# Performance work log

Measured on AMD Instinct MI355X. Metric: run time of the kernel, lower is better.

Reference implementation:

```python
import jax, jax.numpy as jnp
import numpy as np

N = 100000
E = 3200000
F_IN = 128
H1, C1 = 2, 16          # conv1: heads=2, out_channels=16, concat -> 32
H2, C2 = 1, 40          # conv2: heads=1, out_channels=num_classes=40
NEG_SLOPE = 0.2


def setup_inputs() -> dict:
    key = jax.random.key(0)
    ks = jax.random.split(key, 12)
    features = jax.random.normal(ks[0], (N, F_IN), dtype=jnp.float32)
    edges = jax.random.randint(ks[1], (2, E), 0, N, dtype=jnp.int64)
    weight = jax.random.uniform(ks[2], (E,), dtype=jnp.float32)  # ignored (edge_dim=None)
    s = 0.1
    W1 = jax.random.normal(ks[3], (F_IN, H1 * C1), dtype=jnp.float32) * s
    att_src1 = jax.random.normal(ks[4], (H1, C1), dtype=jnp.float32) * s
    att_dst1 = jax.random.normal(ks[5], (H1, C1), dtype=jnp.float32) * s
    b1 = jnp.zeros((H1 * C1,), dtype=jnp.float32)
    W2 = jax.random.normal(ks[6], (H1 * C1, H2 * C2), dtype=jnp.float32) * s
    att_src2 = jax.random.normal(ks[7], (H2, C2), dtype=jnp.float32) * s
    att_dst2 = jax.random.normal(ks[8], (H2, C2), dtype=jnp.float32) * s
    b2 = jnp.zeros((H2 * C2,), dtype=jnp.float32)
    return {"features": features, "edges": edges, "weight": weight,
            "W1": W1, "att_src1": att_src1, "att_dst1": att_dst1, "b1": b1,
            "W2": W2, "att_src2": att_src2, "att_dst2": att_dst2, "b2": b2}


def _segment_softmax(e, seg, num_segments):
    # e: [E, H]; softmax over edges sharing the same destination node
    m = jax.ops.segment_max(e, seg, num_segments=num_segments)
    ex = jnp.exp(e - m[seg])
    s = jax.ops.segment_sum(ex, seg, num_segments=num_segments)
    return ex / (s[seg] + 1e-16)


def _gat_conv(x, src, dst, W, att_src, att_dst, bias, heads, out_ch):
    n = x.shape[0]
    h = (x @ W).reshape(n, heads, out_ch)                  # [N,H,C]
    a_src = jnp.sum(h * att_src, axis=-1)                  # [N,H]
    a_dst = jnp.sum(h * att_dst, axis=-1)                  # [N,H]
    e = a_src[src] + a_dst[dst]                            # [E,H]
    e = jnp.where(e > 0, e, NEG_SLOPE * e)                 # LeakyReLU(0.2)
    alpha = _segment_softmax(e, dst, n)                    # [E,H]
    msg = h[src] * alpha[:, :, None]                       # [E,H,C]
    out = jax.ops.segment_sum(msg, dst, num_segments=n)    # [N,H,C]
    return out.reshape(n, heads * out_ch) + bias           # concat=True


def reference(features, edges, weight, W1, att_src1, att_dst1, b1,
              W2, att_src2, att_dst2, b2):
    n = features.shape[0]
    # GATConv default add_self_loops=True (self-loop removal of pre-existing
    # loops skipped: negligible for random edges and not jit-shape-friendly)
    loop = jnp.arange(n, dtype=edges.dtype)
    src = jnp.concatenate([edges[0], loop])
    dst = jnp.concatenate([edges[1], loop])
    x = _gat_conv(features, src, dst, W1, att_src1, att_dst1, b1, H1, C1)
    x = jax.nn.relu(x)
    # F.dropout with training=self.training -> identity in eval mode
    x = _gat_conv(x, src, dst, W2, att_src2, att_dst2, b2, H2, C2)
    return x
```

## Files before the change

kernel.cpp:

```cpp
#include <hip/hip_runtime.h>


#define DEVFN __device__ __forceinline__
#define CB_SHIFT 8
#define CB_SZ 256
#define SC_CHUNK 4096
#define NBMAX 512
#define STASH 12288
#define A2B 240

DEVFN unsigned short f2h(float f) {
  _Float16 h = (_Float16)f;
  unsigned short u;
  __builtin_memcpy(&u, &h, 2);
  return u;
}
DEVFN float h2f(unsigned short u) {
  _Float16 h;
  __builtin_memcpy(&h, &u, 2);
  return (float)h;
}

DEVFN float lrelu(float e) { return e > 0.f ? e : 0.2f * e; }

DEVFN void acc8(float* acc, float x, uint4 u) {
  acc[0] = fmaf(x, h2f(u.x & 0xffff), acc[0]);
  acc[1] = fmaf(x, h2f(u.x >> 16),    acc[1]);
  acc[2] = fmaf(x, h2f(u.y & 0xffff), acc[2]);
  acc[3] = fmaf(x, h2f(u.y >> 16),    acc[3]);
  acc[4] = fmaf(x, h2f(u.z & 0xffff), acc[4]);
  acc[5] = fmaf(x, h2f(u.z >> 16),    acc[5]);
  acc[6] = fmaf(x, h2f(u.w & 0xffff), acc[6]);
  acc[7] = fmaf(x, h2f(u.w >> 16),    acc[7]);
}

DEVFN void read_edge(const long long* eg64, const int* eg32, int is64, int E,
                     int i, int& s, int& d) {
  if (i >= E) { s = d = i - E; return; }
  if (is64) { s = (int)eg64[i]; d = (int)eg64[E + i]; }
  else      { s = eg32[i];      d = eg32[E + i]; }
}

DEVFN int detect64(const int* eg32, int E, int i0, int t) {
  int base = i0;
  if (base > E - 64) base = E - 64;
  if (base < 0) base = 0;
  int i = base + (t & 63);
  unsigned long long m = __ballot((i < E) && (eg32[2 * i + 1] != 0));
  return m == 0ull;
}

__global__ __launch_bounds__(256) void bucket_hist(const long long* eg64,
                                                   const int* eg32,
                                                   int E, int N, int NB2,
                                                   int* __restrict__ bhist) {
  __shared__ int lh[NBMAX];
  int t = threadIdx.x;
  lh[t] = 0; lh[t + 256] = 0;
  int is64 = detect64(eg32, E, 0, t);
  __syncthreads();
  int EN = E + N;
  int step = (int)gridDim.x * 1024;
  for (int base = (int)blockIdx.x * 1024; base < EN; base += step) {
#pragma unroll
    for (int k = 0; k < 4; k++) {
      int i = base + k * 256 + t;
      if (i < EN) {
        int d;
        if (i >= E) d = i - E;
        else d = is64 ? (int)eg64[E + i] : eg32[E + i];
        atomicAdd(&lh[d >> CB_SHIFT], 1);
      }
    }
  }
  __syncthreads();
  if (t < NB2 && lh[t]) atomicAdd(&bhist[t], lh[t]);
  int t2 = t + 256;
  if (t2 < NB2 && lh[t2]) atomicAdd(&bhist[t2], lh[t2]);
}

__global__ void bucket_scan(const int* __restrict__ bhist,
                            int* __restrict__ bscan, int* __restrict__ gcur,
                            int NB2, int EN) {
  __shared__ int buf[2][NBMAX];
  int t = threadIdx.x;
  int v = (t < NB2) ? bhist[t] : 0;
  buf[0][t] = v;
  __syncthreads();
  int pin = 0;
  for (int off = 1; off < NBMAX; off <<= 1) {
    int nv = buf[pin][t] + (t >= off ? buf[pin][t - off] : 0);
    buf[1 - pin][t] = nv;
    pin ^= 1;
    __syncthreads();
  }
  int excl = buf[pin][t] - v;
  if (t < NB2) { bscan[t] = excl; gcur[t] = excl; }
  if (t == NB2) bscan[t] = EN;
}

__global__ __launch_bounds__(256) void chunk_scatter_sorted(
    const long long* eg64, const int* eg32, int E, int N, int NB2,
    int* __restrict__ gcur, int* __restrict__ tmp) {
  __shared__ int lh[NBMAX];
  __shared__ int lscan[NBMAX];
  __shared__ int lpos[NBMAX];
  __shared__ int gbase[NBMAX];
  __shared__ int sbuf[2][NBMAX];
  __shared__ int payl[SC_CHUNK];
  __shared__ unsigned short bktid[SC_CHUNK];
  int t = threadIdx.x;
  int i0 = (int)blockIdx.x * SC_CHUNK;
  int is64 = detect64(eg32, E, i0, t);
  lh[t] = 0; lh[t + 256] = 0;
  __syncthreads();
  int EN = E + N;
  int i1 = i0 + SC_CHUNK; if (i1 > EN) i1 = EN;
  int total = i1 - i0;
  int es[16], ed[16];
#pragma unroll
  for (int bb = 0; bb < 4; bb++) {
#pragma unroll
    for (int k = 0; k < 4; k++) {
      int idx = bb * 4 + k;
      int i = i0 + bb * 1024 + k * 256 + t;
      int s = 0, d = -1;
      if (i < i1) read_edge(eg64, eg32, is64, E, i, s, d);
      es[idx] = s; ed[idx] = d;
    }
  }
#pragma unroll
  for (int j = 0; j < 16; j++)
    if (ed[j] >= 0) atomicAdd(&lh[ed[j] >> CB_SHIFT], 1);
  __syncthreads();
  sbuf[0][t] = lh[t]; sbuf[0][t + 256] = lh[t + 256];
  __syncthreads();
  int pin = 0;
  for (int off = 1; off < NBMAX; off <<= 1) {
    int nv0 = sbuf[pin][t] + (t >= off ? sbuf[pin][t - off] : 0);
    int nv1 = sbuf[pin][t + 256] + sbuf[pin][t + 256 - off];
    __syncthreads();
    sbuf[1 - pin][t] = nv0; sbuf[1 - pin][t + 256] = nv1;
    pin ^= 1;
    __syncthreads();
  }
  lscan[t] = sbuf[pin][t] - lh[t];
  lscan[t + 256] = sbuf[pin][t + 256] - lh[t + 256];
  lpos[t] = lscan[t]; lpos[t + 256] = lscan[t + 256];
  if (t < NB2 && lh[t]) gbase[t] = atomicAdd(&gcur[t], lh[t]);
  int t2 = t + 256;
  if (t2 < NB2 && lh[t2]) gbase[t2] = atomicAdd(&gcur[t2], lh[t2]);
  __syncthreads();
#pragma unroll
  for (int j = 0; j < 16; j++) {
    if (ed[j] >= 0) {
      int b = ed[j] >> CB_SHIFT;
      int sl = atomicAdd(&lpos[b], 1);
      payl[sl] = (es[j] << CB_SHIFT) | (ed[j] & (CB_SZ - 1));
      bktid[sl] = (unsigned short)b;
    }
  }
  __syncthreads();
  for (int j = t; j < total; j += 256) {
    int b = bktid[j];
    tmp[gbase[b] + (j - lscan[b])] = payl[j];
  }
}

__global__ __launch_bounds__(256) void bucket_rp_sort(const int* __restrict__ bscan,
                                                      const int* __restrict__ tmp,
                                                      int* __restrict__ rp,
                                                      int* __restrict__ csr,
                                                      int N, int EN) {
  __shared__ int lc[CB_SZ];
  __shared__ int ps[256];
  __shared__ int lcur[CB_SZ];
  __shared__ int stash[STASH];
  int b = blockIdx.x, t = threadIdx.x;
  lc[t] = 0;
  __syncthreads();
  int w0 = bscan[b];
  int w1 = bscan[b + 1];
  int cnt = w1 - w0;
  bool fit = (cnt <= STASH);
  int p = w0 + t;
  for (; p + 768 < w1; p += 1024) {
    int e0 = tmp[p], e1 = tmp[p + 256], e2 = tmp[p + 512], e3 = tmp[p + 768];
    if (fit) {
      stash[p - w0] = e0; stash[p - w0 + 256] = e1;
      stash[p - w0 + 512] = e2; stash[p - w0 + 768] = e3;
    }
    atomicAdd(&lc[e0 & (CB_SZ - 1)], 1);
    atomicAdd(&lc[e1 & (CB_SZ - 1)], 1);
    atomicAdd(&lc[e2 & (CB_SZ - 1)], 1);
    atomicAdd(&lc[e3 & (CB_SZ - 1)], 1);
  }
  if (p < w1) {
    bool v1 = p + 256 < w1, v2 = p + 512 < w1;
    int q1 = v1 ? p + 256 : p;
    int q2 = v2 ? p + 512 : p;
    int e0 = tmp[p], e1 = tmp[q1], e2 = tmp[q2];
    if (fit) {
      stash[p - w0] = e0;
      if (v1) stash[q1 - w0] = e1;
      if (v2) stash[q2 - w0] = e2;
    }
    atomicAdd(&lc[e0 & (CB_SZ - 1)], 1);
    if (v1) atomicAdd(&lc[e1 & (CB_SZ - 1)], 1);
    if (v2) atomicAdd(&lc[e2 & (CB_SZ - 1)], 1);
  }
  __syncthreads();
  int a = lc[t];
  ps[t] = a;
  __syncthreads();
  for (int off = 1; off < 256; off <<= 1) {
    int v = ps[t];
    int u = (t >= off) ? ps[t - off] : 0;
    __syncthreads();
    ps[t] = v + u;
    __syncthreads();
  }
  int base = w0 + ps[t] - a;
  lcur[t] = base;
  int n0 = b * CB_SZ;
  if (n0 + t < N) rp[n0 + t] = base;
  if (b == (int)gridDim.x - 1 && t == 0) rp[N] = EN;
  __syncthreads();
  if (fit) {
    for (int j = t; j < cnt; j += 256) {
      int e = stash[j];
      int pos = atomicAdd(&lcur[e & (CB_SZ - 1)], 1);
      csr[pos] = e >> CB_SHIFT;
    }
  } else {
    for (int q = w0 + t; q < w1; q += 256) {
      int e = tmp[q];
      int pos = atomicAdd(&lcur[e & (CB_SZ - 1)], 1);
      csr[pos] = e >> CB_SHIFT;
    }
  }
}

__global__ __launch_bounds__(256) void gemm1f(const float* __restrict__ X,
                                              const float* __restrict__ W,
                                              const float* __restrict__ att_s,
                                              const float* __restrict__ att_d,
                                              uint4* __restrict__ h1h,
                                              float* __restrict__ as1,
                                              float* __restrict__ ad1, int N) {
  __shared__ float Wl[128 * 32];
  __shared__ float Asl[32], Adl[32];
  int t = threadIdx.x;
  for (int i = t; i < 1024; i += 256)
    ((float4*)Wl)[i] = ((const float4*)W)[i];
  if (t < 32) { Asl[t] = att_s[t]; Adl[t] = att_d[t]; }
  __syncthreads();
  int n = blockIdx.x * 256 + t;
  if (n >= N) return;
  const float4* X4 = (const float4*)(X + (size_t)n * 128);
  float acc[32];
#pragma unroll
  for (int c = 0; c < 32; c++) acc[c] = 0.f;
  for (int k4 = 0; k4 < 32; k4++) {
    float4 x = X4[k4];
    const float4* w4 = (const float4*)(Wl + k4 * 128);
#pragma unroll
    for (int c4 = 0; c4 < 8; c4++) {
      float4 w0 = w4[c4], w1 = w4[8 + c4], w2 = w4[16 + c4], w3 = w4[24 + c4];
      float* A = acc + c4 * 4;
      A[0] = fmaf(x.x, w0.x, A[0]); A[1] = fmaf(x.x, w0.y, A[1]);
      A[2] = fmaf(x.x, w0.z, A[2]); A[3] = fmaf(x.x, w0.w, A[3]);
      A[0] = fmaf(x.y, w1.x, A[0]); A[1] = fmaf(x.y, w1.y, A[1]);
      A[2] = fmaf(x.y, w1.z, A[2]); A[3] = fmaf(x.y, w1.w, A[3]);
      A[0] = fmaf(x.z, w2.x, A[0]); A[1] = fmaf(x.z, w2.y, A[1]);
      A[2] = fmaf(x.z, w2.z, A[2]); A[3] = fmaf(x.z, w2.w, A[3]);
      A[0] = fmaf(x.w, w3.x, A[0]); A[1] = fmaf(x.w, w3.y, A[1]);
      A[2] = fmaf(x.w, w3.z, A[2]); A[3] = fmaf(x.w, w3.w, A[3]);
    }
  }
  float s0 = 0.f, d0 = 0.f, s1 = 0.f, d1 = 0.f;
#pragma unroll
  for (int c = 0; c < 16; c++) {
    s0 = fmaf(acc[c], Asl[c], s0);
    d0 = fmaf(acc[c], Adl[c], d0);
    s1 = fmaf(acc[16 + c], Asl[16 + c], s1);
    d1 = fmaf(acc[16 + c], Adl[16 + c], d1);
  }
  as1[n * 2] = s0; as1[n * 2 + 1] = s1;
  ad1[n * 2] = d0; ad1[n * 2 + 1] = d1;
#pragma unroll
  for (int j = 0; j < 4; j++) {
    uint4 u;
    u.x = (unsigned)f2h(acc[j * 8 + 0]) | ((unsigned)f2h(acc[j * 8 + 1]) << 16);
    u.y = (unsigned)f2h(acc[j * 8 + 2]) | ((unsigned)f2h(acc[j * 8 + 3]) << 16);
    u.z = (unsigned)f2h(acc[j * 8 + 4]) | ((unsigned)f2h(acc[j * 8 + 5]) << 16);
    u.w = (unsigned)f2h(acc[j * 8 + 6]) | ((unsigned)f2h(acc[j * 8 + 7]) << 16);
    h1h[(size_t)n * 4 + j] = u;
  }
}

__global__ __launch_bounds__(256, 8) void agg1_gemm2(
    const int* __restrict__ rp, const int* __restrict__ csr,
    const float* __restrict__ as, const float* __restrict__ ad,
    const uint4* __restrict__ h1h, const float* __restrict__ b1,
    const float* __restrict__ W2, const float* __restrict__ as2w,
    const float* __restrict__ ad2w, uint4* __restrict__ h2h,
    float* __restrict__ as2, float* __restrict__ ad2, int N) {
  __shared__ float Wl[32 * 40];
  __shared__ float As2l[40], Ad2l[40];
  __shared__ float x1t[16][33];
  __shared__ float h2r[16][41];
  int t = threadIdx.x;
  for (int i = t; i < 320; i += 256)
    ((float4*)Wl)[i] = ((const float4*)W2)[i];
  if (t < 40) { As2l[t] = as2w[t]; Ad2l[t] = ad2w[t]; }
  int nl = t >> 4, r = t & 15;
  int half = r >> 2, cq = r & 3;
  int h = cq >> 1;
  int n = blockIdx.x * 16 + nl;
  float acc[8] = {0, 0, 0, 0, 0, 0, 0, 0};
  float ssum = 0.f;
  if (n < N) {
    int p0 = rp[n], p1 = rp[n + 1];
    float adv = ad[n * 2 + h];
    int p = p0 + half;
    for (; p + 12 < p1; p += 16) {
      int sA = csr[p], sB = csr[p + 4], sC = csr[p + 8], sD = csr[p + 12];
      float eA = as[sA * 2 + h] + adv;
      float eB = as[sB * 2 + h] + adv;
      float eC = as[sC * 2 + h] + adv;
      float eD = as[sD * 2 + h] + adv;
      uint4 uA = h1h[(size_t)sA * 4 + cq];
      uint4 uB = h1h[(size_t)sB * 4 + cq];
      uint4 uC = h1h[(size_t)sC * 4 + cq];
      uint4 uD = h1h[(size_t)sD * 4 + cq];
      float xA = __expf(lrelu(eA));
      float xB = __expf(lrelu(eB));
      float xC = __expf(lrelu(eC));
      float xD = __expf(lrelu(eD));
      ssum += (xA + xB) + (xC + xD);
      acc8(acc, xA, uA);
      acc8(acc, xB, uB);
      acc8(acc, xC, uC);
      acc8(acc, xD, uD);
    }
    if (p < p1) {
      bool vB = p + 4 < p1, vC = p + 8 < p1;
      int pB = vB ? p + 4 : p;
      int pC = vC ? p + 8 : p;
      int sA = csr[p], sB = csr[pB], sC = csr[pC];
      float eA = as[sA * 2 + h] + adv;
      float eB = as[sB * 2 + h] + adv;
      float eC = as[sC * 2 + h] + adv;
      uint4 uA = h1h[(size_t)sA * 4 + cq];
      uint4 uB = h1h[(size_t)sB * 4 + cq];
      uint4 uC = h1h[(size_t)sC * 4 + cq];
      float xA = __expf(lrelu(eA));
      float xB = vB ? __expf(lrelu(eB)) : 0.f;
      float xC = vC ? __expf(lrelu(eC)) : 0.f;
      ssum += xA + xB + xC;
      acc8(acc, xA, uA);
      acc8(acc, xB, uB);
      acc8(acc, xC, uC);
    }
  }
#pragma unroll
  for (int j = 0; j < 8; j++) acc[j] += __shfl_xor(acc[j], 4);
  ssum += __shfl_xor(ssum, 4);
#pragma unroll
  for (int j = 0; j < 8; j++) acc[j] += __shfl_xor(acc[j], 8);
  ssum += __shfl_xor(ssum, 8);
  if (n < N && half == 0) {
    float inv = 1.0f / (ssum + 1e-16f);
    float4 ba = ((const float4*)b1)[cq * 2];
    float4 bb = ((const float4*)b1)[cq * 2 + 1];
    int ch0 = cq * 8;
    x1t[nl][ch0 + 0] = fmaxf(fmaf(acc[0], inv, ba.x), 0.f);
    x1t[nl][ch0 + 1] = fmaxf(fmaf(acc[1], inv, ba.y), 0.f);
    x1t[nl][ch0 + 2] = fmaxf(fmaf(acc[2], inv, ba.z), 0.f);
    x1t[nl][ch0 + 3] = fmaxf(fmaf(acc[3], inv, ba.w), 0.f);
    x1t[nl][ch0 + 4] = fmaxf(fmaf(acc[4], inv, bb.x), 0.f);
    x1t[nl][ch0 + 5] = fmaxf(fmaf(acc[5], inv, bb.y), 0.f);
    x1t[nl][ch0 + 6] = fmaxf(fmaf(acc[6], inv, bb.z), 0.f);
    x1t[nl][ch0 + 7] = fmaxf(fmaf(acc[7], inv, bb.w), 0.f);
  }
  __syncthreads();
  if (n < N && r < 8) {
    float acc2[5] = {0, 0, 0, 0, 0};
    int cb = r * 5;
    for (int k = 0; k < 32; k++) {
      float x = x1t[nl][k];
#pragma unroll
      for (int c = 0; c < 5; c++)
        acc2[c] = fmaf(x, Wl[k * 40 + cb + c], acc2[c]);
    }
    float ss = 0.f, sd = 0.f;
#pragma unroll
    for (int c = 0; c < 5; c++) {
      ss = fmaf(acc2[c], As2l[cb + c], ss);
      sd = fmaf(acc2[c], Ad2l[cb + c], sd);
    }
#pragma unroll
    for (int off = 1; off < 8; off <<= 1) {
      ss += __shfl_xor(ss, off);
      sd += __shfl_xor(sd, off);
    }
    if (r == 0) { as2[n] = ss; ad2[n] = sd; }
#pragma unroll
    for (int c = 0; c < 5; c++) h2r[nl][cb + c] = acc2[c];
  }
  __syncthreads();
  if (n < N && r < 5) {
    const float* hr = h2r[nl] + r * 8;
    uint4 u;
    u.x = (unsigned)f2h(hr[0]) | ((unsigned)f2h(hr[1]) << 16);
    u.y = (unsigned)f2h(hr[2]) | ((unsigned)f2h(hr[3]) << 16);
    u.z = (unsigned)f2h(hr[4]) | ((unsigned)f2h(hr[5]) << 16);
    u.w = (unsigned)f2h(hr[6]) | ((unsigned)f2h(hr[7]) << 16);
    h2h[(size_t)n * 8 + r] = u;
  }
}

__global__ __launch_bounds__(256, 8) void agg2_fused(const int* __restrict__ rp,
                                                     const int* __restrict__ csr,
                                                     const float* __restrict__ as,
                                                     const float* __restrict__ ad,
                                                     const uint4* __restrict__ h2h,
                                                     const float* __restrict__ bias,
                                                     float* __restrict__ outp, int N) {
  __shared__ float part[256][9];
  int t = threadIdx.x;
  int idx = blockIdx.x * A2B + t;
  bool act = (t < A2B) && (idx < N * 20);
  int n = 0, half = 0, cq = 0, p0 = 0, p1 = 0;
  float adv = 0.f;
  if (act) {
    n = idx / 20;
    int rr = idx % 20;
    half = rr / 5;
    cq = rr - half * 5;
    p0 = rp[n]; p1 = rp[n + 1];
    adv = ad[n];
  }
  float acc[8] = {0, 0, 0, 0, 0, 0, 0, 0};
  float ssum = 0.f;
  if (act) {
    int p = p0 + half;
    for (; p + 12 < p1; p += 16) {
      int sA = csr[p], sB = csr[p + 4], sC = csr[p + 8], sD = csr[p + 12];
      float eA = as[sA] + adv;
      float eB = as[sB] + adv;
      float eC = as[sC] + adv;
      float eD = as[sD] + adv;
      uint4 uA = h2h[(size_t)sA * 8 + cq];
      uint4 uB = h2h[(size_t)sB * 8 + cq];
      uint4 uC = h2h[(size_t)sC * 8 + cq];
      uint4 uD = h2h[(size_t)sD * 8 + cq];
      float xA = __expf(lrelu(eA));
      float xB = __expf(lrelu(eB));
      float xC = __expf(lrelu(eC));
      float xD = __expf(lrelu(eD));
      ssum += (xA + xB) + (xC + xD);
      acc8(acc, xA, uA);
      acc8(acc, xB, uB);
      acc8(acc, xC, uC);
      acc8(acc, xD, uD);
    }
    if (p < p1) {
      bool vB = p + 4 < p1, vC = p + 8 < p1;
      int pB = vB ? p + 4 : p;
      int pC = vC ? p + 8 : p;
      int sA = csr[p], sB = csr[pB], sC = csr[pC];
      float eA = as[sA] + adv;
      float eB = as[sB] + adv;
      float eC = as[sC] + adv;
      uint4 uA = h2h[(size_t)sA * 8 + cq];
      uint4 uB = h2h[(size_t)sB * 8 + cq];
      uint4 uC = h2h[(size_t)sC * 8 + cq];
      float xA = __expf(lrelu(eA));
      float xB = vB ? __expf(lrelu(eB)) : 0.f;
      float xC = vC ? __expf(lrelu(eC)) : 0.f;
      ssum += xA + xB + xC;
      acc8(acc, xA, uA);
      acc8(acc, xB, uB);
      acc8(acc, xC, uC);
    }
  }
  if (act && half) {
#pragma unroll
    for (int j = 0; j < 8; j++) part[t][j] = acc[j];
    part[t][8] = ssum;
  }
  __syncthreads();
  if (act && half == 0) {
#pragma unroll
    for (int j = 0; j < 8; j++)
      acc[j] += part[t + 5][j] + part[t + 10][j] + part[t + 15][j];
    ssum += part[t + 5][8] + part[t + 10][8] + part[t + 15][8];
    float inv = 1.0f / (ssum + 1e-16f);
    const float4* b4 = (const float4*)bias;
    float4 ba = b4[cq * 2], bb = b4[cq * 2 + 1];
    float4 r0, r1;
    r0.x = fmaf(acc[0], inv, ba.x);
    r0.y = fmaf(acc[1], inv, ba.y);
    r0.z = fmaf(acc[2], inv, ba.z);
    r0.w = fmaf(acc[3], inv, ba.w);
    r1.x = fmaf(acc[4], inv, bb.x);
    r1.y = fmaf(acc[5], inv, bb.y);
    r1.z = fmaf(acc[6], inv, bb.z);
    r1.w = fmaf(acc[7], inv, bb.w);
    ((float4*)outp)[(size_t)n * 10 + cq * 2]     = r0;
    ((float4*)outp)[(size_t)n * 10 + cq * 2 + 1] = r1;
  }
}

extern "C" void kernel_launch(void* const* d_in, const int* in_sizes, int n_in,
                              void* d_out, int out_size, void* d_ws, size_t ws_size,
                              hipStream_t stream) {
  const float* X    = (const float*)d_in[0];
  const long long* eg64 = (const long long*)d_in[1];
  const int* eg32   = (const int*)d_in[1];
  const float* W1   = (const float*)d_in[3];
  const float* as1w = (const float*)d_in[4];
  const float* ad1w = (const float*)d_in[5];
  const float* b1   = (const float*)d_in[6];
  const float* W2   = (const float*)d_in[7];
  const float* as2w = (const float*)d_in[8];
  const float* ad2w = (const float*)d_in[9];
  const float* b2   = (const float*)d_in[10];
  float* out = (float*)d_out;

  const int N  = in_sizes[0] / 128;
  const int E  = in_sizes[1] / 2;
  const int EN = E + N;
  const int NB2 = (N + CB_SZ - 1) / CB_SZ;
  const int NWG = (EN + SC_CHUNK - 1) / SC_CHUNK;

  char* wbase = (char*)d_ws;
  size_t off = 0;
  auto alloc = [&](size_t bytes) -> void* {
    void* p = wbase + off;
    off += (bytes + 255) & ~(size_t)255;
    return p;
  };

  uint4* h1h = (uint4*)alloc((size_t)N * 64);
  size_t usz = (size_t)EN * 4;
  if ((size_t)N * 128 > usz) usz = (size_t)N * 128;
  char* uni = (char*)alloc(usz);
  uint4* h2h = (uint4*)uni;
  int*   tmp = (int*)uni;
  float* as1 = (float*)alloc((size_t)N * 2 * 4);
  float* ad1 = (float*)alloc((size_t)N * 2 * 4);
  float* as2 = (float*)alloc((size_t)N * 4);
  float* ad2 = (float*)alloc((size_t)N * 4);
  int* rp     = (int*)alloc((size_t)(N + 1) * 4);
  int* bhist  = (int*)alloc(NBMAX * 4);
  int* bscan  = (int*)alloc((NBMAX + 1) * 4);
  int* gcur   = (int*)alloc(NBMAX * 4);
  int* csr    = (int*)alloc((size_t)EN * 4);
  (void)ws_size; (void)n_in; (void)out_size;

  const int gN = (N + 255) / 256;

  hipMemsetAsync(bhist, 0, NBMAX * 4, stream);
  bucket_hist<<<1024, 256, 0, stream>>>(eg64, eg32, E, N, NB2, bhist);
  bucket_scan<<<1, NBMAX, 0, stream>>>(bhist, bscan, gcur, NB2, EN);
  chunk_scatter_sorted<<<NWG, 256, 0, stream>>>(eg64, eg32, E, N, NB2, gcur, tmp);
  bucket_rp_sort<<<NB2, 256, 0, stream>>>(bscan, tmp, rp, csr, N, EN);

  gemm1f<<<gN, 256, 0, stream>>>(X, W1, as1w, ad1w, h1h, as1, ad1, N);
  agg1_gemm2<<<(N + 15) / 16, 256, 0, stream>>>(rp, csr, as1, ad1, h1h, b1,
                                                W2, as2w, ad2w, h2h, as2, ad2, N);
  agg2_fused<<<(N * 20 + A2B - 1) / A2B, 256, 0, stream>>>(rp, csr, as2, ad2,
                                                           h2h, b2, out, N);
}
```

Measured before the change: 331.7 us.

## Replace per-bucket CSR sort with global per-node histogram, scan, and atomic scatter

The CSR build no longer does a bucket histogram followed by a per-bucket block sort that stashes each bucket in LDS. It now counts every destination node with global atomics, runs a three-kernel prefix scan to produce row pointers and bucket cursors, keeps the chunked bucket scatter (which also writes bucket ids), and finishes with a flat atomic scatter into CSR positions. This removes the per-bucket LDS-limited sort kernel, whose per-block work depended on bucket size. In exchange it adds global atomic contention on per-node counters, extra launches, an extra bucket-id array written and read, and a full per-node memset.

Result: slower. 491.0 us (+48.0%).

```diff
diff --git a/kernel.cpp b/kernel.cpp
--- a/kernel.cpp
+++ b/kernel.cpp
@@ -6,7 +6,6 @@
 #define CB_SZ 256
 #define SC_CHUNK 4096
 #define NBMAX 512
-#define STASH 12288
 #define A2B 240
 
 DEVFN unsigned short f2h(float f) {
@@ -50,58 +49,90 @@
   return m == 0ull;
 }
 
-__global__ __launch_bounds__(256) void bucket_hist(const long long* eg64,
-                                                   const int* eg32,
-                                                   int E, int N, int NB2,
-                                                   int* __restrict__ bhist) {
-  __shared__ int lh[NBMAX];
-  int t = threadIdx.x;
-  lh[t] = 0; lh[t + 256] = 0;
+__global__ __launch_bounds__(256) void node_hist(const long long* eg64,
+                                                 const int* eg32,
+                                                 int E, int N,
+                                                 int* __restrict__ ncnt) {
+  int t = threadIdx.x;
   int is64 = detect64(eg32, E, 0, t);
-  __syncthreads();
   int EN = E + N;
-  int step = (int)gridDim.x * 1024;
-  for (int base = (int)blockIdx.x * 1024; base < EN; base += step) {
-#pragma unroll
-    for (int k = 0; k < 4; k++) {
-      int i = base + k * 256 + t;
-      if (i < EN) {
-        int d;
-        if (i >= E) d = i - E;
-        else d = is64 ? (int)eg64[E + i] : eg32[E + i];
-        atomicAdd(&lh[d >> CB_SHIFT], 1);
-      }
-    }
-  }
-  __syncthreads();
-  if (t < NB2 && lh[t]) atomicAdd(&bhist[t], lh[t]);
-  int t2 = t + 256;
-  if (t2 < NB2 && lh[t2]) atomicAdd(&bhist[t2], lh[t2]);
-}
-
-__global__ void bucket_scan(const int* __restrict__ bhist,
-                            int* __restrict__ bscan, int* __restrict__ gcur,
-                            int NB2, int EN) {
-  __shared__ int buf[2][NBMAX];
-  int t = threadIdx.x;
-  int v = (t < NB2) ? bhist[t] : 0;
+  int base = (int)blockIdx.x * 1024 + t;
+#pragma unroll
+  for (int k = 0; k < 4; k++) {
+    int i = base + k * 256;
+    if (i < EN) {
+      int d;
+      if (i >= E) d = i - E;
+      else d = is64 ? (int)eg64[E + i] : eg32[E + i];
+      atomicAdd(&ncnt[d], 1);
+    }
+  }
+}
+
+__global__ void scan_blocks(const int* __restrict__ cnt, int* __restrict__ rp,
+                            int* __restrict__ bsum, int n) {
+  __shared__ int buf[2][1024];
+  int t = threadIdx.x;
+  int gid = blockIdx.x * 1024 + t;
+  int v = (gid < n) ? cnt[gid] : 0;
   buf[0][t] = v;
   __syncthreads();
   int pin = 0;
-  for (int off = 1; off < NBMAX; off <<= 1) {
-    int nv = buf[pin][t] + (t >= off ? buf[pin][t - off] : 0);
+  for (int offd = 1; offd < 1024; offd <<= 1) {
+    int nv = buf[pin][t];
+    if (t >= offd) nv += buf[pin][t - offd];
     buf[1 - pin][t] = nv;
-    pin ^= 1;
+    pin = 1 - pin;
     __syncthreads();
   }
-  int excl = buf[pin][t] - v;
-  if (t < NB2) { bscan[t] = excl; gcur[t] = excl; }
-  if (t == NB2) bscan[t] = EN;
+  int inc = buf[pin][t];
+  if (gid < n) rp[gid] = inc - v;
+  if (t == 1023) bsum[blockIdx.x] = inc;
+}
+
+__global__ void scan_sums(const int* __restrict__ bsum, int* __restrict__ boff,
+                          int nb) {
+  __shared__ int buf[2][1024];
+  __shared__ int carry;
+  int t = threadIdx.x;
+  if (t == 0) carry = 0;
+  __syncthreads();
+  for (int base = 0; base < nb; base += 1024) {
+    int v = (base + t < nb) ? bsum[base + t] : 0;
+    buf[0][t] = v;
+    __syncthreads();
+    int pin = 0;
+    for (int off = 1; off < 1024; off <<= 1) {
+      int nv = buf[pin][t];
+      if (t >= off) nv += buf[pin][t - off];
+      buf[1 - pin][t] = nv;
+      pin = 1 - pin;
+      __syncthreads();
+    }
+    if (base + t < nb) boff[base + t] = carry + buf[pin][t] - v;
+    __syncthreads();
+    if (t == 0) carry += buf[pin][1023];
+    __syncthreads();
+  }
+}
+
+__global__ void scan_add_init(int* __restrict__ rp, const int* __restrict__ boff,
+                              int* __restrict__ ncur, int* __restrict__ gcur,
+                              int n, int total) {
+  int i = blockIdx.x * 1024 + threadIdx.x;
+  if (i < n) {
+    int v = rp[i] + boff[blockIdx.x];
+    rp[i] = v;
+    ncur[i] = v;
+    if ((i & (CB_SZ - 1)) == 0) gcur[i >> CB_SHIFT] = v;
+  }
+  if (i == 0) rp[n] = total;
 }
 
 __global__ __launch_bounds__(256) void chunk_scatter_sorted(
     const long long* eg64, const int* eg32, int E, int N, int NB2,
-    int* __restrict__ gcur, int* __restrict__ tmp) {
+    int* __restrict__ gcur, int* __restrict__ tmp,
+    unsigned short* __restrict__ tmpb) {
   __shared__ int lh[NBMAX];
   __shared__ int lscan[NBMAX];
   __shared__ int lpos[NBMAX];
@@ -163,79 +194,24 @@
   __syncthreads();
   for (int j = t; j < total; j += 256) {
     int b = bktid[j];
-    tmp[gbase[b] + (j - lscan[b])] = payl[j];
-  }
-}
-
-__global__ __launch_bounds__(256) void bucket_rp_sort(const int* __restrict__ bscan,
-                                                      const int* __restrict__ tmp,
-                                                      int* __restrict__ rp,
-                                                      int* __restrict__ csr,
-                                                      int N, int EN) {
-  __shared__ int lc[CB_SZ];
-  __shared__ int ps[256];
-  __shared__ int lcur[CB_SZ];
-  __shared__ int stash[STASH];
-  int b = blockIdx.x, t = threadIdx.x;
-  lc[t] = 0;
-  __syncthreads();
-  int w0 = bscan[b];
-  int w1 = bscan[b + 1];
-  int cnt = w1 - w0;
-  bool fit = (cnt <= STASH);
-  int p = w0 + t;
-  for (; p + 768 < w1; p += 1024) {
-    int e0 = tmp[p], e1 = tmp[p + 256], e2 = tmp[p + 512], e3 = tmp[p + 768];
-    if (fit) {
-      stash[p - w0] = e0; stash[p - w0 + 256] = e1;
-      stash[p - w0 + 512] = e2; stash[p - w0 + 768] = e3;
-    }
-    atomicAdd(&lc[e0 & (CB_SZ - 1)], 1);
-    atomicAdd(&lc[e1 & (CB_SZ - 1)], 1);
-    atomicAdd(&lc[e2 & (CB_SZ - 1)], 1);
-    atomicAdd(&lc[e3 & (CB_SZ - 1)], 1);
-  }
-  if (p < w1) {
-    bool v1 = p + 256 < w1, v2 = p + 512 < w1;
-    int q1 = v1 ? p + 256 : p;
-    int q2 = v2 ? p + 512 : p;
-    int e0 = tmp[p], e1 = tmp[q1], e2 = tmp[q2];
-    if (fit) {
-      stash[p - w0] = e0;
-      if (v1) stash[q1 - w0] = e1;
-      if (v2) stash[q2 - w0] = e2;
-    }
-    atomicAdd(&lc[e0 & (CB_SZ - 1)], 1);
-    if (v1) atomicAdd(&lc[e1 & (CB_SZ - 1)], 1);
-    if (v2) atomicAdd(&lc[e2 & (CB_SZ - 1)], 1);
-  }
-  __syncthreads();
-  int a = lc[t];
-  ps[t] = a;
-  __syncthreads();
-  for (int off = 1; off < 256; off <<= 1) {
-    int v = ps[t];
-    int u = (t >= off) ? ps[t - off] : 0;
-    __syncthreads();
-    ps[t] = v + u;
-    __syncthreads();
-  }
-  int base = w0 + ps[t] - a;
-  lcur[t] = base;
-  int n0 = b * CB_SZ;
-  if (n0 + t < N) rp[n0 + t] = base;
-  if (b == (int)gridDim.x - 1 && t == 0) rp[N] = EN;
-  __syncthreads();
-  if (fit) {
-    for (int j = t; j < cnt; j += 256) {
-      int e = stash[j];
-      int pos = atomicAdd(&lcur[e & (CB_SZ - 1)], 1);
-      csr[pos] = e >> CB_SHIFT;
-    }
-  } else {
-    for (int q = w0 + t; q < w1; q += 256) {
-      int e = tmp[q];
-      int pos = atomicAdd(&lcur[e & (CB_SZ - 1)], 1);
+    int dstp = gbase[b] + (j - lscan[b]);
+    tmp[dstp] = payl[j];
+    tmpb[dstp] = (unsigned short)b;
+  }
+}
+
+__global__ __launch_bounds__(256) void csr_scatter(const int* __restrict__ tmp,
+                                                   const unsigned short* __restrict__ tmpb,
+                                                   int* __restrict__ ncur,
+                                                   int* __restrict__ csr, int EN) {
+  int base = (int)blockIdx.x * 1024 + threadIdx.x;
+#pragma unroll
+  for (int k = 0; k < 4; k++) {
+    int i = base + k * 256;
+    if (i < EN) {
+      int e = tmp[i];
+      int node = ((int)tmpb[i] << CB_SHIFT) | (e & (CB_SZ - 1));
+      int pos = atomicAdd(&ncur[node], 1);
       csr[pos] = e >> CB_SHIFT;
     }
   }
@@ -535,6 +511,8 @@
   const int EN = E + N;
   const int NB2 = (N + CB_SZ - 1) / CB_SZ;
   const int NWG = (EN + SC_CHUNK - 1) / SC_CHUNK;
+  const int NWE = (EN + 1023) / 1024;
+  const int nbS = (N + 1023) / 1024;
 
   char* wbase = (char*)d_ws;
   size_t off = 0;
@@ -550,24 +528,30 @@
   char* uni = (char*)alloc(usz);
   uint4* h2h = (uint4*)uni;
   int*   tmp = (int*)uni;
+  unsigned short* tmpb = (unsigned short*)alloc((size_t)EN * 2);
   float* as1 = (float*)alloc((size_t)N * 2 * 4);
   float* ad1 = (float*)alloc((size_t)N * 2 * 4);
   float* as2 = (float*)alloc((size_t)N * 4);
   float* ad2 = (float*)alloc((size_t)N * 4);
   int* rp     = (int*)alloc((size_t)(N + 1) * 4);
-  int* bhist  = (int*)alloc(NBMAX * 4);
-  int* bscan  = (int*)alloc((NBMAX + 1) * 4);
+  int* ncnt   = (int*)alloc((size_t)N * 4);
+  int* ncur   = (int*)alloc((size_t)N * 4);
   int* gcur   = (int*)alloc(NBMAX * 4);
+  int* bsum   = (int*)alloc(1024 * 4);
+  int* boff   = (int*)alloc(1024 * 4);
   int* csr    = (int*)alloc((size_t)EN * 4);
   (void)ws_size; (void)n_in; (void)out_size;
 
   const int gN = (N + 255) / 256;
 
-  hipMemsetAsync(bhist, 0, NBMAX * 4, stream);
-  bucket_hist<<<1024, 256, 0, stream>>>(eg64, eg32, E, N, NB2, bhist);
-  bucket_scan<<<1, NBMAX, 0, stream>>>(bhist, bscan, gcur, NB2, EN);
-  chunk_scatter_sorted<<<NWG, 256, 0, stream>>>(eg64, eg32, E, N, NB2, gcur, tmp);
-  bucket_rp_sort<<<NB2, 256, 0, stream>>>(bscan, tmp, rp, csr, N, EN);
+  hipMemsetAsync(ncnt, 0, (size_t)N * 4, stream);
+  node_hist<<<NWE, 256, 0, stream>>>(eg64, eg32, E, N, ncnt);
+  scan_blocks<<<nbS, 1024, 0, stream>>>(ncnt, rp, bsum, N);
+  scan_sums<<<1, 1024, 0, stream>>>(bsum, boff, nbS);
+  scan_add_init<<<nbS, 1024, 0, stream>>>(rp, boff, ncur, gcur, N, EN);
+  chunk_scatter_sorted<<<NWG, 256, 0, stream>>>(eg64, eg32, E, N, NB2, gcur,
+                                                tmp, tmpb);
+  csr_scatter<<<NWE, 256, 0, stream>>>(tmp, tmpb, ncur, csr, EN);
 
   gemm1f<<<gN, 256, 0, stream>>>(X, W1, as1w, ad1w, h1h, as1, ad1, N);
   agg1_gemm2<<<(N + 15) / 16, 256, 0, stream>>>(rp, csr, as1, ad1, h1h, b1,
```

## Aggregate layer-2 on 32-channel inputs and apply W2 after aggregation

Applied to the files above, without the earlier changes.

Layer 2 now gathers the 32-channel fp16 hidden vector x1 instead of the 40-channel projected h2, because aggregation is linear: sum(alpha*x1)@W2 equals sum(alpha*x1@W2). The layer-2 attention scores are computed from x1 through precomputed vectors W2·att_src2 and W2·att_dst2, so the first aggregation kernel no longer does the small GEMM. The second kernel aggregates with the same 16-thread-per-node layout as layer 1, then applies W2 and the bias per node. This cuts gathered bytes per edge from 80 to 64 and reduces the workspace, at the cost of a small GEMM in the final kernel and a slightly different fp16 rounding point.

Result: faster. 323.3 us (-2.6%).

```diff
diff --git a/kernel.cpp b/kernel.cpp
--- a/kernel.cpp
+++ b/kernel.cpp
@@ -7,7 +7,6 @@
 #define SC_CHUNK 4096
 #define NBMAX 512
 #define STASH 12288
-#define A2B 240
 
 DEVFN unsigned short f2h(float f) {
   _Float16 h = (_Float16)f;
@@ -299,21 +298,25 @@
   }
 }
 
-__global__ __launch_bounds__(256, 8) void agg1_gemm2(
+__global__ __launch_bounds__(256, 8) void agg1_attn(
     const int* __restrict__ rp, const int* __restrict__ csr,
     const float* __restrict__ as, const float* __restrict__ ad,
     const uint4* __restrict__ h1h, const float* __restrict__ b1,
     const float* __restrict__ W2, const float* __restrict__ as2w,
-    const float* __restrict__ ad2w, uint4* __restrict__ h2h,
+    const float* __restrict__ ad2w, uint4* __restrict__ x1h,
     float* __restrict__ as2, float* __restrict__ ad2, int N) {
-  __shared__ float Wl[32 * 40];
-  __shared__ float As2l[40], Ad2l[40];
-  __shared__ float x1t[16][33];
-  __shared__ float h2r[16][41];
+  __shared__ float val[32], vbl[32];
   int t = threadIdx.x;
-  for (int i = t; i < 320; i += 256)
-    ((float4*)Wl)[i] = ((const float4*)W2)[i];
-  if (t < 40) { As2l[t] = as2w[t]; Ad2l[t] = ad2w[t]; }
+  if (t < 32) {
+    float a = 0.f, b = 0.f;
+    for (int c = 0; c < 40; c++) {
+      float w = W2[t * 40 + c];
+      a = fmaf(w, as2w[c], a);
+      b = fmaf(w, ad2w[c], b);
+    }
+    val[t] = a; vbl[t] = b;
+  }
+  __syncthreads();
   int nl = t >> 4, r = t & 15;
   int half = r >> 2, cq = r & 3;
   int h = cq >> 1;
@@ -374,77 +377,53 @@
     float inv = 1.0f / (ssum + 1e-16f);
     float4 ba = ((const float4*)b1)[cq * 2];
     float4 bb = ((const float4*)b1)[cq * 2 + 1];
+    float xv[8];
+    xv[0] = fmaxf(fmaf(acc[0], inv, ba.x), 0.f);
+    xv[1] = fmaxf(fmaf(acc[1], inv, ba.y), 0.f);
+    xv[2] = fmaxf(fmaf(acc[2], inv, ba.z), 0.f);
+    xv[3] = fmaxf(fmaf(acc[3], inv, ba.w), 0.f);
+    xv[4] = fmaxf(fmaf(acc[4], inv, bb.x), 0.f);
+    xv[5] = fmaxf(fmaf(acc[5], inv, bb.y), 0.f);
+    xv[6] = fmaxf(fmaf(acc[6], inv, bb.z), 0.f);
+    xv[7] = fmaxf(fmaf(acc[7], inv, bb.w), 0.f);
+    uint4 u;
+    u.x = (unsigned)f2h(xv[0]) | ((unsigned)f2h(xv[1]) << 16);
+    u.y = (unsigned)f2h(xv[2]) | ((unsigned)f2h(xv[3]) << 16);
+    u.z = (unsigned)f2h(xv[4]) | ((unsigned)f2h(xv[5]) << 16);
+    u.w = (unsigned)f2h(xv[6]) | ((unsigned)f2h(xv[7]) << 16);
+    x1h[(size_t)n * 4 + cq] = u;
     int ch0 = cq * 8;
-    x1t[nl][ch0 + 0] = fmaxf(fmaf(acc[0], inv, ba.x), 0.f);
-    x1t[nl][ch0 + 1] = fmaxf(fmaf(acc[1], inv, ba.y), 0.f);
-    x1t[nl][ch0 + 2] = fmaxf(fmaf(acc[2], inv, ba.z), 0.f);
-    x1t[nl][ch0 + 3] = fmaxf(fmaf(acc[3], inv, ba.w), 0.f);
-    x1t[nl][ch0 + 4] = fmaxf(fmaf(acc[4], inv, bb.x), 0.f);
-    x1t[nl][ch0 + 5] = fmaxf(fmaf(acc[5], inv, bb.y), 0.f);
-    x1t[nl][ch0 + 6] = fmaxf(fmaf(acc[6], inv, bb.z), 0.f);
-    x1t[nl][ch0 + 7] = fmaxf(fmaf(acc[7], inv, bb.w), 0.f);
-  }
-  __syncthreads();
-  if (n < N && r < 8) {
-    float acc2[5] = {0, 0, 0, 0, 0};
-    int cb = r * 5;
-    for (int k = 0; k < 32; k++) {
-      float x = x1t[nl][k];
-#pragma unroll
-      for (int c = 0; c < 5; c++)
-        acc2[c] = fmaf(x, Wl[k * 40 + cb + c], acc2[c]);
-    }
     float ss = 0.f, sd = 0.f;
 #pragma unroll
-    for (int c = 0; c < 5; c++) {
-      ss = fmaf(acc2[c], As2l[cb + c], ss);
-      sd = fmaf(acc2[c], Ad2l[cb + c], sd);
-    }
-#pragma unroll
-    for (int off = 1; off < 8; off <<= 1) {
-      ss += __shfl_xor(ss, off);
-      sd += __shfl_xor(sd, off);
-    }
-    if (r == 0) { as2[n] = ss; ad2[n] = sd; }
-#pragma unroll
-    for (int c = 0; c < 5; c++) h2r[nl][cb + c] = acc2[c];
-  }
-  __syncthreads();
-  if (n < N && r < 5) {
-    const float* hr = h2r[nl] + r * 8;
-    uint4 u;
-    u.x = (unsigned)f2h(hr[0]) | ((unsigned)f2h(hr[1]) << 16);
-    u.y = (unsigned)f2h(hr[2]) | ((unsigned)f2h(hr[3]) << 16);
-    u.z = (unsigned)f2h(hr[4]) | ((unsigned)f2h(hr[5]) << 16);
-    u.w = (unsigned)f2h(hr[6]) | ((unsigned)f2h(hr[7]) << 16);
-    h2h[(size_t)n * 8 + r] = u;
-  }
-}
-
-__global__ __launch_bounds__(256, 8) void agg2_fused(const int* __restrict__ rp,
-                                                     const int* __restrict__ csr,
-                                                     const float* __restrict__ as,
-                                                     const float* __restrict__ ad,
-                                                     const uint4* __restrict__ h2h,
-                                                     const float* __restrict__ bias,
-                                                     float* __restrict__ outp, int N) {
-  __shared__ float part[256][9];
+    for (int j = 0; j < 8; j++) {
+      ss = fmaf(xv[j], val[ch0 + j], ss);
+      sd = fmaf(xv[j], vbl[ch0 + j], sd);
+    }
+    ss += __shfl_xor(ss, 1); sd += __shfl_xor(sd, 1);
+    ss += __shfl_xor(ss, 2); sd += __shfl_xor(sd, 2);
+    if (cq == 0) { as2[n] = ss; ad2[n] = sd; }
+  }
+}
+
+__global__ __launch_bounds__(256, 8) void agg2_gemm(
+    const int* __restrict__ rp, const int* __restrict__ csr,
+    const float* __restrict__ as, const float* __restrict__ ad,
+    const uint4* __restrict__ x1h, const float* __restrict__ W2,
+    const float* __restrict__ b2, float* __restrict__ outp, int N) {
+  __shared__ float Wl[32 * 40];
+  __shared__ float xt[16][33];
+  __shared__ float hr[16][41];
   int t = threadIdx.x;
-  int idx = blockIdx.x * A2B + t;
-  bool act = (t < A2B) && (idx < N * 20);
-  int n = 0, half = 0, cq = 0, p0 = 0, p1 = 0;
-  float adv = 0.f;
-  if (act) {
-    n = idx / 20;
-    int rr = idx % 20;
-    half = rr / 5;
-    cq = rr - half * 5;
-    p0 = rp[n]; p1 = rp[n + 1];
-    adv = ad[n];
-  }
+  for (int i = t; i < 320; i += 256)
+    ((float4*)Wl)[i] = ((const float4*)W2)[i];
+  int nl = t >> 4, r = t & 15;
+  int half = r >> 2, cq = r & 3;
+  int n = blockIdx.x * 16 + nl;
   float acc[8] = {0, 0, 0, 0, 0, 0, 0, 0};
   float ssum = 0.f;
-  if (act) {
+  if (n < N) {
+    int p0 = rp[n], p1 = rp[n + 1];
+    float adv = ad[n];
     int p = p0 + half;
     for (; p + 12 < p1; p += 16) {
       int sA = csr[p], sB = csr[p + 4], sC = csr[p + 8], sD = csr[p + 12];
@@ -452,10 +431,10 @@
       float eB = as[sB] + adv;
       float eC = as[sC] + adv;
       float eD = as[sD] + adv;
-      uint4 uA = h2h[(size_t)sA * 8 + cq];
-      uint4 uB = h2h[(size_t)sB * 8 + cq];
-      uint4 uC = h2h[(size_t)sC * 8 + cq];
-      uint4 uD = h2h[(size_t)sD * 8 + cq];
+      uint4 uA = x1h[(size_t)sA * 4 + cq];
+      uint4 uB = x1h[(size_t)sB * 4 + cq];
+      uint4 uC = x1h[(size_t)sC * 4 + cq];
+      uint4 uD = x1h[(size_t)sD * 4 + cq];
       float xA = __expf(lrelu(eA));
       float xB = __expf(lrelu(eB));
       float xC = __expf(lrelu(eC));
@@ -474,9 +453,9 @@
       float eA = as[sA] + adv;
       float eB = as[sB] + adv;
       float eC = as[sC] + adv;
-      uint4 uA = h2h[(size_t)sA * 8 + cq];
-      uint4 uB = h2h[(size_t)sB * 8 + cq];
-      uint4 uC = h2h[(size_t)sC * 8 + cq];
+      uint4 uA = x1h[(size_t)sA * 4 + cq];
+      uint4 uB = x1h[(size_t)sB * 4 + cq];
+      uint4 uC = x1h[(size_t)sC * 4 + cq];
       float xA = __expf(lrelu(eA));
       float xB = vB ? __expf(lrelu(eB)) : 0.f;
       float xC = vC ? __expf(lrelu(eC)) : 0.f;
@@ -486,31 +465,39 @@
       acc8(acc, xC, uC);
     }
   }
-  if (act && half) {
-#pragma unroll
-    for (int j = 0; j < 8; j++) part[t][j] = acc[j];
-    part[t][8] = ssum;
-  }
-  __syncthreads();
-  if (act && half == 0) {
-#pragma unroll
-    for (int j = 0; j < 8; j++)
-      acc[j] += part[t + 5][j] + part[t + 10][j] + part[t + 15][j];
-    ssum += part[t + 5][8] + part[t + 10][8] + part[t + 15][8];
+#pragma unroll
+  for (int j = 0; j < 8; j++) acc[j] += __shfl_xor(acc[j], 4);
+  ssum += __shfl_xor(ssum, 4);
+#pragma unroll
+  for (int j = 0; j < 8; j++) acc[j] += __shfl_xor(acc[j], 8);
+  ssum += __shfl_xor(ssum, 8);
+  if (n < N && half == 0) {
     float inv = 1.0f / (ssum + 1e-16f);
-    const float4* b4 = (const float4*)bias;
-    float4 ba = b4[cq * 2], bb = b4[cq * 2 + 1];
-    float4 r0, r1;
-    r0.x = fmaf(acc[0], inv, ba.x);
-    r0.y = fmaf(acc[1], inv, ba.y);
-    r0.z = fmaf(acc[2], inv, ba.z);
-    r0.w = fmaf(acc[3], inv, ba.w);
-    r1.x = fmaf(acc[4], inv, bb.x);
-    r1.y = fmaf(acc[5], inv, bb.y);
-    r1.z = fmaf(acc[6], inv, bb.z);
-    r1.w = fmaf(acc[7], inv, bb.w);
-    ((float4*)outp)[(size_t)n * 10 + cq * 2]     = r0;
-    ((float4*)outp)[(size_t)n * 10 + cq * 2 + 1] = r1;
+    int ch0 = cq * 8;
+#pragma unroll
+    for (int j = 0; j < 8; j++) xt[nl][ch0 + j] = acc[j] * inv;
+  }
+  __syncthreads();
+  if (n < N && r < 8) {
+    float a2[5] = {0, 0, 0, 0, 0};
+    int cb = r * 5;
+    for (int k = 0; k < 32; k++) {
+      float x = xt[nl][k];
+#pragma unroll
+      for (int c = 0; c < 5; c++)
+        a2[c] = fmaf(x, Wl[k * 40 + cb + c], a2[c]);
+    }
+#pragma unroll
+    for (int c = 0; c < 5; c++) hr[nl][cb + c] = a2[c];
+  }
+  __syncthreads();
+  if (n < N && r < 10) {
+    const float* s = hr[nl] + r * 4;
+    float4 bb = ((const float4*)b2)[r];
+    float4 v;
+    v.x = s[0] + bb.x; v.y = s[1] + bb.y;
+    v.z = s[2] + bb.z; v.w = s[3] + bb.w;
+    ((float4*)outp)[(size_t)n * 10 + r] = v;
   }
 }
 
@@ -546,9 +533,9 @@
 
   uint4* h1h = (uint4*)alloc((size_t)N * 64);
   size_t usz = (size_t)EN * 4;
-  if ((size_t)N * 128 > usz) usz = (size_t)N * 128;
+  if ((size_t)N * 64 > usz) usz = (size_t)N * 64;
   char* uni = (char*)alloc(usz);
-  uint4* h2h = (uint4*)uni;
+  uint4* x1h = (uint4*)uni;
   int*   tmp = (int*)uni;
   float* as1 = (float*)alloc((size_t)N * 2 * 4);
   float* ad1 = (float*)alloc((size_t)N * 2 * 4);
@@ -570,8 +557,8 @@
   bucket_rp_sort<<<NB2, 256, 0, stream>>>(bscan, tmp, rp, csr, N, EN);
 
   gemm1f<<<gN, 256, 0, stream>>>(X, W1, as1w, ad1w, h1h, as1, ad1, N);
-  agg1_gemm2<<<(N + 15) / 16, 256, 0, stream>>>(rp, csr, as1, ad1, h1h, b1,
-                                                W2, as2w, ad2w, h2h, as2, ad2, N);
-  agg2_fused<<<(N * 20 + A2B - 1) / A2B, 256, 0, stream>>>(rp, csr, as2, ad2,
-                                                           h2h, b2, out, N);
-}
+  agg1_attn<<<(N + 15) / 16, 256, 0, stream>>>(rp, csr, as1, ad1, h1h, b1,
+                                               W2, as2w, ad2w, x1h, as2, ad2, N);
+  agg2_gemm<<<(N + 15) / 16, 256, 0, stream>>>(rp, csr, as2, ad2, x1h,
+                                               W2, b2, out, N);
+}
```
